# Performance work log

Hardware: AMD Instinct MI355X
Metric: run time of the kernel (lower is better)

Reference implementation:

```python
import jax, jax.numpy as jnp
import numpy as np

N_NODES = 100000
N_EDGES = 3200000


def spmm(row, col, val, x):
    # out[i] = sum_{e: row[e]==i} val[e] * x[col[e]]  -- sparse adj @ x
    return jax.ops.segment_sum(val[:, None] * x[col], row, num_segments=N_NODES)


def setup_inputs() -> dict:
    key = jax.random.key(0)
    k1, k2, k3, k4, k5, k6 = jax.random.split(key, 6)
    out_feat, hid_feat, in_feat = 32, 64, 128
    # xavier_uniform bounds
    b1 = float(np.sqrt(6.0 / (out_feat + hid_feat)))
    b2 = float(np.sqrt(6.0 / (hid_feat + in_feat)))
    return {
        "feat": jax.random.normal(k1, (N_NODES, out_feat), dtype=jnp.float32),
        "W1": jax.random.uniform(k2, (out_feat, hid_feat), minval=-b1, maxval=b1, dtype=jnp.float32),
        "W2": jax.random.uniform(k3, (hid_feat, in_feat), minval=-b2, maxval=b2, dtype=jnp.float32),
        "edge_row": jax.random.randint(k4, (N_EDGES,), 0, N_NODES, dtype=jnp.int32),
        "edge_col": jax.random.randint(k5, (N_EDGES,), 0, N_NODES, dtype=jnp.int32),
        "edge_val": jax.random.uniform(k6, (N_EDGES,), dtype=jnp.float32),
    }


def reference(feat, W1, W2, edge_row, edge_col, edge_val):
    x = feat @ W1                                  # [N, hid]
    x = spmm(edge_row, edge_col, edge_val, x)      # adj @ x
    # add_act=False: no activation
    x = x @ W2                                     # [N, in_feat]
    x = spmm(edge_row, edge_col, edge_val, x)      # adj @ x
    return x
```

## Files before the change

### kernel.cpp

```cpp
#include <hip/hip_runtime.h>

#define N_NODES 100000
#define N_EDGES 3200000
#define RPB 128
#define NB ((N_NODES + RPB - 1) / RPB)

typedef unsigned short ushort_t;
typedef unsigned int uint_t;

__device__ __forceinline__ ushort_t f32_to_bf16_rne(float f) {
    uint_t b = __float_as_uint(f);
    return (ushort_t)((b + 0x7FFFu + ((b >> 16) & 1u)) >> 16);
}
__device__ __forceinline__ float bf16_lo(uint_t u) {
    return __uint_as_float(u << 16);
}
__device__ __forceinline__ float bf16_hi(uint_t u) {
    return __uint_as_float(u & 0xffff0000u);
}


__global__ void gemm_w12_kernel(const float* __restrict__ W1,
                                const float* __restrict__ W2,
                                float* __restrict__ W12) {
    int idx = blockIdx.x * blockDim.x + threadIdx.x;
    if (idx >= 32 * 128) return;
    int r = idx >> 7;
    int c = idx & 127;
    float acc = 0.f;
#pragma unroll
    for (int k = 0; k < 64; ++k) acc += W1[r * 64 + k] * W2[k * 128 + c];
    W12[idx] = acc;
}

__global__ void cvt_bf16_kernel(const float* __restrict__ in, ushort_t* __restrict__ ob) {
    int i = blockIdx.x * blockDim.x + threadIdx.x;
    if (i < N_NODES * 32) ob[i] = f32_to_bf16_rne(in[i]);
}

__global__ void gemm_out_kernel(const float* __restrict__ g2,
                                const float* __restrict__ W12,
                                float* __restrict__ out) {
    int tid = threadIdx.x;
    int jo = (tid & 31) * 4;
    int rl = tid >> 5;
    float4 w[32];
#pragma unroll
    for (int k = 0; k < 32; ++k) w[k] = *(const float4*)&W12[k * 128 + jo];
    for (int r = blockIdx.x * 8 + rl; r < N_NODES; r += gridDim.x * 8) {
        const float4* g4 = (const float4*)(g2 + (size_t)r * 32);
        float4 acc = make_float4(0.f, 0.f, 0.f, 0.f);
#pragma unroll
        for (int q = 0; q < 8; ++q) {
            float4 gv = g4[q];
            int k = q * 4;
            acc.x += gv.x * w[k].x;     acc.y += gv.x * w[k].y;
            acc.z += gv.x * w[k].z;     acc.w += gv.x * w[k].w;
            acc.x += gv.y * w[k + 1].x; acc.y += gv.y * w[k + 1].y;
            acc.z += gv.y * w[k + 1].z; acc.w += gv.y * w[k + 1].w;
            acc.x += gv.z * w[k + 2].x; acc.y += gv.z * w[k + 2].y;
            acc.z += gv.z * w[k + 2].z; acc.w += gv.z * w[k + 2].w;
            acc.x += gv.w * w[k + 3].x; acc.y += gv.w * w[k + 3].y;
            acc.z += gv.w * w[k + 3].z; acc.w += gv.w * w[k + 3].w;
        }
        *(float4*)&out[(size_t)r * 128 + jo] = acc;
    }
}


__global__ void hist_bucket_kernel(const int* __restrict__ row, int* __restrict__ cnt) {
    __shared__ int h[NB];
    for (int t = threadIdx.x; t < NB; t += blockDim.x) h[t] = 0;
    __syncthreads();
    int per = (N_EDGES + gridDim.x - 1) / gridDim.x;
    int s = blockIdx.x * per;
    int e = min(s + per, N_EDGES);
    for (int i = s + threadIdx.x; i < e; i += blockDim.x)
        atomicAdd(&h[row[i] >> 7], 1);
    __syncthreads();
    for (int t = threadIdx.x; t < NB; t += blockDim.x)
        if (h[t]) atomicAdd(&cnt[t], h[t]);
}

__global__ void scan_bucket_kernel(const int* __restrict__ cnt,
                                   int* __restrict__ offs, int* __restrict__ cur_b) {
    __shared__ int s[1024];
    int t = threadIdx.x;
    int v = (t < NB) ? cnt[t] : 0;
    s[t] = v;
    __syncthreads();
    for (int off = 1; off < 1024; off <<= 1) {
        int add = (t >= off) ? s[t - off] : 0;
        __syncthreads();
        s[t] += add;
        __syncthreads();
    }
    if (t < NB) { int x = s[t] - v; offs[t] = x; cur_b[t] = x; }
    if (t == 0) offs[NB] = N_EDGES;
}

__global__ void scatter_bucket_kernel(const int* __restrict__ row, const int* __restrict__ col,
                                      const float* __restrict__ val,
                                      int* __restrict__ cur_b, int2* __restrict__ ebuf) {
    __shared__ int h[NB];
    __shared__ int base[NB];
    for (int t = threadIdx.x; t < NB; t += blockDim.x) h[t] = 0;
    __syncthreads();
    int per = (N_EDGES + gridDim.x - 1) / gridDim.x;
    int s = blockIdx.x * per;
    int e = min(s + per, N_EDGES);
    for (int i = s + threadIdx.x; i < e; i += blockDim.x)
        atomicAdd(&h[row[i] >> 7], 1);
    __syncthreads();
    for (int t = threadIdx.x; t < NB; t += blockDim.x) {
        int c = h[t];
        base[t] = c ? atomicAdd(&cur_b[t], c) : 0;
        h[t] = 0;
    }
    __syncthreads();
    for (int i = s + threadIdx.x; i < e; i += blockDim.x) {
        int r = row[i];
        int b = r >> 7;
        int lp = atomicAdd(&h[b], 1);
        ebuf[base[b] + lp] = make_int2((col[i] << 7) | (r & 127), __float_as_int(val[i]));
    }
}

__global__ void rowsort_kernel(const int* __restrict__ offs, const int2* __restrict__ ebuf,
                               int2* __restrict__ ep, int* __restrict__ rs) {
    __shared__ int h[RPB];
    __shared__ int loff[RPB];
    __shared__ int curl[RPB];
    int b = blockIdx.x;
    int s = offs[b], e = offs[b + 1];
    int t = threadIdx.x;
    if (t < RPB) h[t] = 0;
    __syncthreads();
    for (int i = s + t; i < e; i += blockDim.x)
        atomicAdd(&h[ebuf[i].x & 127], 1);
    __syncthreads();
    if (t < RPB) loff[t] = h[t];
    __syncthreads();
    for (int off = 1; off < RPB; off <<= 1) {
        int add = (t < RPB && t >= off) ? loff[t - off] : 0;
        __syncthreads();
        if (t < RPB) loff[t] += add;
        __syncthreads();
    }
    if (t < RPB) {
        int excl = loff[t] - h[t];
        curl[t] = excl;
        int r = b * RPB + t;
        if (r < N_NODES) rs[r] = s + excl;
    }
    if (b == 0 && t == 0) rs[N_NODES] = N_EDGES;
    __syncthreads();
    for (int i = s + t; i < e; i += blockDim.x) {
        int2 cv = ebuf[i];
        int rl = cv.x & 127;
        int pos = s + atomicAdd(&curl[rl], 1);
        ep[pos] = make_int2(cv.x >> 7, cv.y);
    }
}

template <bool OUT_BF16>
__global__ void spmm_csr_kernel(const int* __restrict__ rs,
                                const int2* __restrict__ ep,
                                const uint_t* __restrict__ xb,
                                void* __restrict__ outv) {
    int gid = blockIdx.x * blockDim.x + threadIdx.x;
    int wid = gid >> 6;
    int nwaves = (gridDim.x * blockDim.x) >> 6;
    int lane = threadIdx.x & 63;
    int j2 = lane & 15;
    int g = lane >> 4;
    for (int r = wid; r < N_NODES; r += nwaves) {
        int s = rs[r], e = rs[r + 1];
        float a0 = 0.f, a1 = 0.f, b0 = 0.f, b1 = 0.f;
        int p = s + g;
        for (; p + 28 < e; p += 32) {
            int2 c0 = ep[p];
            int2 c1 = ep[p + 4];
            int2 c2 = ep[p + 8];
            int2 c3 = ep[p + 12];
            int2 c4 = ep[p + 16];
            int2 c5 = ep[p + 20];
            int2 c6 = ep[p + 24];
            int2 c7 = ep[p + 28];
            uint_t u0 = xb[c0.x * 16 + j2];
            uint_t u1 = xb[c1.x * 16 + j2];
            uint_t u2 = xb[c2.x * 16 + j2];
            uint_t u3 = xb[c3.x * 16 + j2];
            uint_t u4 = xb[c4.x * 16 + j2];
            uint_t u5 = xb[c5.x * 16 + j2];
            uint_t u6 = xb[c6.x * 16 + j2];
            uint_t u7 = xb[c7.x * 16 + j2];
            float w0 = __int_as_float(c0.y);
            float w1 = __int_as_float(c1.y);
            float w2 = __int_as_float(c2.y);
            float w3 = __int_as_float(c3.y);
            float w4 = __int_as_float(c4.y);
            float w5 = __int_as_float(c5.y);
            float w6 = __int_as_float(c6.y);
            float w7 = __int_as_float(c7.y);
            a0 += w0 * bf16_lo(u0); a1 += w0 * bf16_hi(u0);
            b0 += w1 * bf16_lo(u1); b1 += w1 * bf16_hi(u1);
            a0 += w2 * bf16_lo(u2); a1 += w2 * bf16_hi(u2);
            b0 += w3 * bf16_lo(u3); b1 += w3 * bf16_hi(u3);
            a0 += w4 * bf16_lo(u4); a1 += w4 * bf16_hi(u4);
            b0 += w5 * bf16_lo(u5); b1 += w5 * bf16_hi(u5);
            a0 += w6 * bf16_lo(u6); a1 += w6 * bf16_hi(u6);
            b0 += w7 * bf16_lo(u7); b1 += w7 * bf16_hi(u7);
        }
        for (; p < e; p += 4) {
            int2 cv = ep[p];
            uint_t u = xb[cv.x * 16 + j2];
            float w = __int_as_float(cv.y);
            a0 += w * bf16_lo(u);
            a1 += w * bf16_hi(u);
        }
        float r0 = a0 + b0;
        float r1 = a1 + b1;
        r0 += __shfl_xor(r0, 16, 64);
        r0 += __shfl_xor(r0, 32, 64);
        r1 += __shfl_xor(r1, 16, 64);
        r1 += __shfl_xor(r1, 32, 64);
        if (g == 0) {
            if constexpr (OUT_BF16) {
                uint_t pk = (uint_t)f32_to_bf16_rne(r0) | ((uint_t)f32_to_bf16_rne(r1) << 16);
                ((uint_t*)outv)[r * 16 + j2] = pk;
            } else {
                ((float2*)outv)[r * 16 + j2] = make_float2(r0, r1);
            }
        }
    }
}

__global__ void spmm32_atomic_kernel(const int* __restrict__ row,
                                     const int* __restrict__ col,
                                     const float* __restrict__ val,
                                     const float* __restrict__ x,
                                     float* __restrict__ out) {
    int id = blockIdx.x * blockDim.x + threadIdx.x;
    int e = id >> 5;
    int j = id & 31;
    if (e >= N_EDGES) return;
    atomicAdd(&out[row[e] * 32 + j], val[e] * x[col[e] * 32 + j]);
}

__global__ void gemm_out_fallback_kernel(const float* __restrict__ g2,
                                         const float* __restrict__ W12,
                                         float* __restrict__ out) {
    int id = blockIdx.x * blockDim.x + threadIdx.x;
    int i = id >> 7;
    int j = id & 127;
    const float* g = g2 + i * 32;
    float acc = 0.f;
#pragma unroll
    for (int k = 0; k < 32; ++k) acc += g[k] * W12[k * 128 + j];
    out[id] = acc;
}

extern "C" void kernel_launch(void* const* d_in, const int* in_sizes, int n_in,
                              void* d_out, int out_size, void* d_ws, size_t ws_size,
                              hipStream_t stream) {
    const float* feat = (const float*)d_in[0];
    const float* W1   = (const float*)d_in[1];
    const float* W2   = (const float*)d_in[2];
    const int*   erow = (const int*)d_in[3];
    const int*   ecol = (const int*)d_in[4];
    const float* eval_= (const float*)d_in[5];
    float* out = (float*)d_out;

    float*    W12   = (float*)d_ws;
    ushort_t* xb    = (ushort_t*)(W12 + 4096);
    ushort_t* g1b   = xb + (size_t)N_NODES * 32;
    float*    g2    = (float*)(g1b + (size_t)N_NODES * 32);
    int2*     ep    = (int2*)(g2 + (size_t)N_NODES * 32);
    int*      cnt   = (int*)(ep + N_EDGES);
    int*      offs  = cnt + NB;
    int*      cur_b = offs + NB + 1;
    int*      rs    = cur_b + NB;
    size_t    needed = (size_t)((char*)(rs + N_NODES + 2) - (char*)d_ws);

    int2* ebuf = (int2*)d_out;

    gemm_w12_kernel<<<16, 256, 0, stream>>>(W1, W2, W12);

    if (ws_size >= needed) {
        cvt_bf16_kernel<<<(N_NODES * 32 + 255) / 256, 256, 0, stream>>>(feat, xb);

        hipMemsetAsync(cnt, 0, NB * sizeof(int), stream);
        hist_bucket_kernel<<<256, 1024, 0, stream>>>(erow, cnt);
        scan_bucket_kernel<<<1, 1024, 0, stream>>>(cnt, offs, cur_b);
        scatter_bucket_kernel<<<256, 1024, 0, stream>>>(erow, ecol, eval_, cur_b, ebuf);
        rowsort_kernel<<<NB, 512, 0, stream>>>(offs, ebuf, ep, rs);

        spmm_csr_kernel<true><<<2048, 256, 0, stream>>>(rs, ep, (const uint_t*)xb, g1b);
        spmm_csr_kernel<false><<<2048, 256, 0, stream>>>(rs, ep, (const uint_t*)g1b, g2);

        gemm_out_kernel<<<1024, 256, 0, stream>>>(g2, W12, out);
    } else {
        float* g1f = (float*)d_ws + 4096;
        float* g2f = g1f + (size_t)N_NODES * 32;
        hipMemsetAsync(g1f, 0, (size_t)N_NODES * 32 * 2 * sizeof(float), stream);
        spmm32_atomic_kernel<<<(N_EDGES * 32) / 256, 256, 0, stream>>>(erow, ecol, eval_, feat, g1f);
        spmm32_atomic_kernel<<<(N_EDGES * 32) / 256, 256, 0, stream>>>(erow, ecol, eval_, g1f, g2f);
        gemm_out_fallback_kernel<<<(N_NODES * 128) / 256, 256, 0, stream>>>(g2f, W12, out);
    }
}
```

Measured before the change: 269.8 us.

## Split SpMM by column half to keep gathered feature rows cache-resident

The row sort now also partitions each row's edges by whether the column index falls in the lower or upper half of nodes, and records a per-row midpoint. Each SpMM runs as two passes, each gathering from only half of the feature matrix, so the gathered working set (about 3.2MB of bf16 per half) is more likely to stay in L2/MALL. The second pass adds the first pass's fp32 partials. Edge-list loads become nontemporal, a 4-wide unrolled tail loop is added, and the histogram and scatter grids are doubled. The cost is reading the edge list twice per SpMM plus an extra read and write of the fp32 partial array.

After: 349.7 us. 29.6% more time.

```diff
diff --git a/kernel.cpp b/kernel.cpp
--- a/kernel.cpp
+++ b/kernel.cpp
@@ -4,6 +4,7 @@
 #define N_EDGES 3200000
 #define RPB 128
 #define NB ((N_NODES + RPB - 1) / RPB)
+#define CHALF 50000
 
 typedef unsigned short ushort_t;
 typedef unsigned int uint_t;
@@ -127,47 +128,56 @@
 }
 
 __global__ void rowsort_kernel(const int* __restrict__ offs, const int2* __restrict__ ebuf,
-                               int2* __restrict__ ep, int* __restrict__ rs) {
-    __shared__ int h[RPB];
-    __shared__ int loff[RPB];
-    __shared__ int curl[RPB];
+                               int2* __restrict__ ep, int* __restrict__ rs,
+                               int* __restrict__ mid) {
+    __shared__ int h[RPB * 2];
+    __shared__ int loff[RPB * 2];
+    __shared__ int curl[RPB * 2];
     int b = blockIdx.x;
     int s = offs[b], e = offs[b + 1];
     int t = threadIdx.x;
-    if (t < RPB) h[t] = 0;
-    __syncthreads();
-    for (int i = s + t; i < e; i += blockDim.x)
-        atomicAdd(&h[ebuf[i].x & 127], 1);
-    __syncthreads();
-    if (t < RPB) loff[t] = h[t];
-    __syncthreads();
-    for (int off = 1; off < RPB; off <<= 1) {
-        int add = (t < RPB && t >= off) ? loff[t - off] : 0;
-        __syncthreads();
-        if (t < RPB) loff[t] += add;
-        __syncthreads();
-    }
-    if (t < RPB) {
-        int excl = loff[t] - h[t];
-        curl[t] = excl;
-        int r = b * RPB + t;
-        if (r < N_NODES) rs[r] = s + excl;
-    }
-    if (b == 0 && t == 0) rs[N_NODES] = N_EDGES;
+    if (t < RPB * 2) h[t] = 0;
     __syncthreads();
     for (int i = s + t; i < e; i += blockDim.x) {
         int2 cv = ebuf[i];
-        int rl = cv.x & 127;
-        int pos = s + atomicAdd(&curl[rl], 1);
+        int k = ((cv.x & 127) << 1) | ((cv.x >> 7) >= CHALF ? 1 : 0);
+        atomicAdd(&h[k], 1);
+    }
+    __syncthreads();
+    if (t < RPB * 2) loff[t] = h[t];
+    __syncthreads();
+    for (int off = 1; off < RPB * 2; off <<= 1) {
+        int add = (t < RPB * 2 && t >= off) ? loff[t - off] : 0;
+        __syncthreads();
+        if (t < RPB * 2) loff[t] += add;
+        __syncthreads();
+    }
+    if (t < RPB * 2) curl[t] = loff[t] - h[t];
+    __syncthreads();
+    if (t < RPB) {
+        int r = b * RPB + t;
+        if (r < N_NODES) {
+            rs[r]  = s + curl[2 * t];
+            mid[r] = s + curl[2 * t + 1];
+        }
+    }
+    if (b == 0 && t == 0) rs[N_NODES] = N_EDGES;
+    __syncthreads();
+    for (int i = s + t; i < e; i += blockDim.x) {
+        int2 cv = ebuf[i];
+        int k = ((cv.x & 127) << 1) | ((cv.x >> 7) >= CHALF ? 1 : 0);
+        int pos = s + atomicAdd(&curl[k], 1);
         ep[pos] = make_int2(cv.x >> 7, cv.y);
     }
 }
 
-template <bool OUT_BF16>
-__global__ void spmm_csr_kernel(const int* __restrict__ rs,
-                                const int2* __restrict__ ep,
-                                const uint_t* __restrict__ xb,
-                                void* __restrict__ outv) {
+template <int PASS, bool OUT_BF16>
+__global__ void spmm_split_kernel(const int* __restrict__ rs,
+                                  const int* __restrict__ mid,
+                                  const long long* __restrict__ ep,
+                                  const uint_t* __restrict__ xb,
+                                  const float2* __restrict__ part,
+                                  void* __restrict__ outv) {
     int gid = blockIdx.x * blockDim.x + threadIdx.x;
     int wid = gid >> 6;
     int nwaves = (gridDim.x * blockDim.x) >> 6;
@@ -175,34 +185,35 @@
     int j2 = lane & 15;
     int g = lane >> 4;
     for (int r = wid; r < N_NODES; r += nwaves) {
-        int s = rs[r], e = rs[r + 1];
+        int lo = (PASS == 0) ? rs[r] : mid[r];
+        int hi = (PASS == 0) ? mid[r] : rs[r + 1];
         float a0 = 0.f, a1 = 0.f, b0 = 0.f, b1 = 0.f;
-        int p = s + g;
-        for (; p + 28 < e; p += 32) {
-            int2 c0 = ep[p];
-            int2 c1 = ep[p + 4];
-            int2 c2 = ep[p + 8];
-            int2 c3 = ep[p + 12];
-            int2 c4 = ep[p + 16];
-            int2 c5 = ep[p + 20];
-            int2 c6 = ep[p + 24];
-            int2 c7 = ep[p + 28];
-            uint_t u0 = xb[c0.x * 16 + j2];
-            uint_t u1 = xb[c1.x * 16 + j2];
-            uint_t u2 = xb[c2.x * 16 + j2];
-            uint_t u3 = xb[c3.x * 16 + j2];
-            uint_t u4 = xb[c4.x * 16 + j2];
-            uint_t u5 = xb[c5.x * 16 + j2];
-            uint_t u6 = xb[c6.x * 16 + j2];
-            uint_t u7 = xb[c7.x * 16 + j2];
-            float w0 = __int_as_float(c0.y);
-            float w1 = __int_as_float(c1.y);
-            float w2 = __int_as_float(c2.y);
-            float w3 = __int_as_float(c3.y);
-            float w4 = __int_as_float(c4.y);
-            float w5 = __int_as_float(c5.y);
-            float w6 = __int_as_float(c6.y);
-            float w7 = __int_as_float(c7.y);
+        int p = lo + g;
+        for (; p + 28 < hi; p += 32) {
+            long long v0 = __builtin_nontemporal_load(ep + p);
+            long long v1 = __builtin_nontemporal_load(ep + p + 4);
+            long long v2 = __builtin_nontemporal_load(ep + p + 8);
+            long long v3 = __builtin_nontemporal_load(ep + p + 12);
+            long long v4 = __builtin_nontemporal_load(ep + p + 16);
+            long long v5 = __builtin_nontemporal_load(ep + p + 20);
+            long long v6 = __builtin_nontemporal_load(ep + p + 24);
+            long long v7 = __builtin_nontemporal_load(ep + p + 28);
+            uint_t u0 = xb[(int)(v0 & 0xffffffffLL) * 16 + j2];
+            uint_t u1 = xb[(int)(v1 & 0xffffffffLL) * 16 + j2];
+            uint_t u2 = xb[(int)(v2 & 0xffffffffLL) * 16 + j2];
+            uint_t u3 = xb[(int)(v3 & 0xffffffffLL) * 16 + j2];
+            uint_t u4 = xb[(int)(v4 & 0xffffffffLL) * 16 + j2];
+            uint_t u5 = xb[(int)(v5 & 0xffffffffLL) * 16 + j2];
+            uint_t u6 = xb[(int)(v6 & 0xffffffffLL) * 16 + j2];
+            uint_t u7 = xb[(int)(v7 & 0xffffffffLL) * 16 + j2];
+            float w0 = __int_as_float((int)(v0 >> 32));
+            float w1 = __int_as_float((int)(v1 >> 32));
+            float w2 = __int_as_float((int)(v2 >> 32));
+            float w3 = __int_as_float((int)(v3 >> 32));
+            float w4 = __int_as_float((int)(v4 >> 32));
+            float w5 = __int_as_float((int)(v5 >> 32));
+            float w6 = __int_as_float((int)(v6 >> 32));
+            float w7 = __int_as_float((int)(v7 >> 32));
             a0 += w0 * bf16_lo(u0); a1 += w0 * bf16_hi(u0);
             b0 += w1 * bf16_lo(u1); b1 += w1 * bf16_hi(u1);
             a0 += w2 * bf16_lo(u2); a1 += w2 * bf16_hi(u2);
@@ -212,10 +223,28 @@
             a0 += w6 * bf16_lo(u6); a1 += w6 * bf16_hi(u6);
             b0 += w7 * bf16_lo(u7); b1 += w7 * bf16_hi(u7);
         }
-        for (; p < e; p += 4) {
-            int2 cv = ep[p];
-            uint_t u = xb[cv.x * 16 + j2];
-            float w = __int_as_float(cv.y);
+        for (; p + 12 < hi; p += 16) {
+            long long v0 = __builtin_nontemporal_load(ep + p);
+            long long v1 = __builtin_nontemporal_load(ep + p + 4);
+            long long v2 = __builtin_nontemporal_load(ep + p + 8);
+            long long v3 = __builtin_nontemporal_load(ep + p + 12);
+            uint_t u0 = xb[(int)(v0 & 0xffffffffLL) * 16 + j2];
+            uint_t u1 = xb[(int)(v1 & 0xffffffffLL) * 16 + j2];
+            uint_t u2 = xb[(int)(v2 & 0xffffffffLL) * 16 + j2];
+            uint_t u3 = xb[(int)(v3 & 0xffffffffLL) * 16 + j2];
+            float w0 = __int_as_float((int)(v0 >> 32));
+            float w1 = __int_as_float((int)(v1 >> 32));
+            float w2 = __int_as_float((int)(v2 >> 32));
+            float w3 = __int_as_float((int)(v3 >> 32));
+            a0 += w0 * bf16_lo(u0); a1 += w0 * bf16_hi(u0);
+            b0 += w1 * bf16_lo(u1); b1 += w1 * bf16_hi(u1);
+            a0 += w2 * bf16_lo(u2); a1 += w2 * bf16_hi(u2);
+            b0 += w3 * bf16_lo(u3); b1 += w3 * bf16_hi(u3);
+        }
+        for (; p < hi; p += 4) {
+            long long v = __builtin_nontemporal_load(ep + p);
+            uint_t u = xb[(int)(v & 0xffffffffLL) * 16 + j2];
+            float w = __int_as_float((int)(v >> 32));
             a0 += w * bf16_lo(u);
             a1 += w * bf16_hi(u);
         }
@@ -226,7 +255,14 @@
         r1 += __shfl_xor(r1, 16, 64);
         r1 += __shfl_xor(r1, 32, 64);
         if (g == 0) {
-            if constexpr (OUT_BF16) {
+            if (PASS == 1) {
+                float2 pv = part[r * 16 + j2];
+                r0 += pv.x;
+                r1 += pv.y;
+            }
+            if (PASS == 0) {
+                ((float2*)outv)[r * 16 + j2] = make_float2(r0, r1);
+            } else if constexpr (OUT_BF16) {
                 uint_t pk = (uint_t)f32_to_bf16_rne(r0) | ((uint_t)f32_to_bf16_rne(r1) << 16);
                 ((uint_t*)outv)[r * 16 + j2] = pk;
             } else {
@@ -281,7 +317,8 @@
     int*      offs  = cnt + NB;
     int*      cur_b = offs + NB + 1;
     int*      rs    = cur_b + NB;
-    size_t    needed = (size_t)((char*)(rs + N_NODES + 2) - (char*)d_ws);
+    int*      mid   = rs + N_NODES + 2;
+    size_t    needed = (size_t)((char*)(mid + N_NODES) - (char*)d_ws);
 
     int2* ebuf = (int2*)d_out;
 
@@ -291,13 +328,16 @@
         cvt_bf16_kernel<<<(N_NODES * 32 + 255) / 256, 256, 0, stream>>>(feat, xb);
 
         hipMemsetAsync(cnt, 0, NB * sizeof(int), stream);
-        hist_bucket_kernel<<<256, 1024, 0, stream>>>(erow, cnt);
+        hist_bucket_kernel<<<512, 1024, 0, stream>>>(erow, cnt);
         scan_bucket_kernel<<<1, 1024, 0, stream>>>(cnt, offs, cur_b);
-        scatter_bucket_kernel<<<256, 1024, 0, stream>>>(erow, ecol, eval_, cur_b, ebuf);
-        rowsort_kernel<<<NB, 512, 0, stream>>>(offs, ebuf, ep, rs);
-
-        spmm_csr_kernel<true><<<2048, 256, 0, stream>>>(rs, ep, (const uint_t*)xb, g1b);
-        spmm_csr_kernel<false><<<2048, 256, 0, stream>>>(rs, ep, (const uint_t*)g1b, g2);
+        scatter_bucket_kernel<<<512, 1024, 0, stream>>>(erow, ecol, eval_, cur_b, ebuf);
+        rowsort_kernel<<<NB, 512, 0, stream>>>(offs, ebuf, ep, rs, mid);
+
+        const long long* epl = (const long long*)ep;
+        spmm_split_kernel<0, false><<<2048, 256, 0, stream>>>(rs, mid, epl, (const uint_t*)xb, nullptr, g2);
+        spmm_split_kernel<1, true ><<<2048, 256, 0, stream>>>(rs, mid, epl, (const uint_t*)xb, (const float2*)g2, g1b);
+        spmm_split_kernel<0, false><<<2048, 256, 0, stream>>>(rs, mid, epl, (const uint_t*)g1b, nullptr, g2);
+        spmm_split_kernel<1, false><<<2048, 256, 0, stream>>>(rs, mid, epl, (const uint_t*)g1b, (const float2*)g2, g2);
 
         gemm_out_kernel<<<1024, 256, 0, stream>>>(g2, W12, out);
     } else {
```
